# Performance work log

Measured on AMD Instinct MI355X. Metric: run time of the kernel, lower is better.

The kernel has to match this reference:

```python
import jax, jax.numpy as jnp
import numpy as np
import math

B, T = 8, 16
CODE_NUM = 1024
CODE_SIZE = 48
GRAPH_SIZE = 32
HIDDEN = 150      # hidden_size == t_output_size
T_ATTN = 32       # t_attention_size
DP_ATTN = 32      # DotProductAttention size
OUT = 1024


def _lin(k, fan_in, fan_out):
    s = 1.0 / math.sqrt(fan_in)
    kw, kb = jax.random.split(k)
    W = jax.random.uniform(kw, (fan_in, fan_out), minval=-s, maxval=s, dtype=jnp.float32)
    b = jax.random.uniform(kb, (fan_out,), minval=-s, maxval=s, dtype=jnp.float32)
    return W, b


def setup_inputs():
    key = jax.random.key(0)
    ks = jax.random.split(key, 16)
    u = jax.random.uniform(ks[0], (B, T, CODE_NUM))
    m1 = (u < 0.03).astype(jnp.float32)                   # persistent codes
    m2 = ((u >= 0.03) & (u < 0.05)).astype(jnp.float32)   # emerging neighbor codes
    m3 = ((u >= 0.05) & (u < 0.06)).astype(jnp.float32)   # emerging unrelated codes
    divided = jnp.stack([m1, m2, m3], axis=-1)            # [B,T,N,3], disjoint
    code_x = jnp.clip(m1 + m2 + m3, 0.0, 1.0)             # current-visit codes
    neighbors = ((u >= 0.06) & (u < 0.12)).astype(jnp.float32)
    lens = jax.random.randint(ks[1], (B,), T // 2, T + 1)
    a = (jax.random.uniform(ks[2], (CODE_NUM, CODE_NUM)) < 0.01).astype(jnp.float32)
    adj = a / (a.sum(axis=1, keepdims=True) + 1e-6)
    c_emb = jax.random.normal(ks[3], (CODE_NUM, CODE_SIZE)) * 0.05
    n_emb = jax.random.normal(ks[4], (CODE_NUM, CODE_SIZE)) * 0.05
    u_emb = jax.random.normal(ks[5], (CODE_NUM, GRAPH_SIZE)) * 0.05
    Wg, bg = _lin(ks[6], CODE_SIZE, GRAPH_SIZE)           # GraphLayer dense
    Wi, bi = _lin(ks[7], GRAPH_SIZE, 3 * HIDDEN)          # GRUCell input (r|z|n)
    Wh, bh = _lin(ks[8], HIDDEN, 3 * HIDDEN)              # GRUCell hidden (r|z|n)
    Wq, bq = _lin(ks[9], GRAPH_SIZE, T_ATTN)
    Wk, bk = _lin(ks[10], GRAPH_SIZE, T_ATTN)
    Wv, bv = _lin(ks[11], GRAPH_SIZE, HIDDEN)
    Wd, bd = _lin(ks[12], HIDDEN, DP_ATTN)                # DotProductAttention dense
    context = jax.random.normal(ks[13], (DP_ATTN,)) * 0.1
    Wc, bc = _lin(ks[14], HIDDEN, OUT)                    # Classifier
    return dict(code_x=code_x, divided=divided, neighbors=neighbors, lens=lens,
                adj=adj, c_emb=c_emb, n_emb=n_emb, u_emb=u_emb, Wg=Wg, bg=bg,
                Wi=Wi, bi=bi, Wh=Wh, bh=bh, Wq=Wq, bq=bq, Wk=Wk, bk=bk,
                Wv=Wv, bv=bv, Wd=Wd, bd=bd, context=context, Wc=Wc, bc=bc)


def _forward(code_x, divided, neighbors, lens, adj, c_emb, n_emb, u_emb,
             Wg, bg, Wi, bi, Wh, bh, Wq, bq, Wk, bk, Wv, bv, Wd, bd, context, Wc, bc):
    Bb, Tt, N = code_x.shape
    H = Wh.shape[0]
    NEG = -1e30
    scale = 1.0 / math.sqrt(Wq.shape[1])

    def step(carry, xs):
        h_prev, no_prev = carry                 # [B,N,H], [B,N,G]
        c_t, d_t, n_t, t_idx = xs               # [B,N], [B,N,3], [B,N], scalar
        c = c_t[..., None]
        nb = n_t[..., None]
        # GraphLayer: masked embeddings + one-hop adjacency aggregation
        ce = c * c_emb                           # [B,N,C]
        ne = nb * n_emb
        adj_ce = jnp.einsum('mn,bnc->bmc', adj, ce)
        adj_ne = jnp.einsum('mn,bnc->bmc', adj, ne)
        co = jax.nn.leaky_relu((ce + c * adj_ce + c * adj_ne) @ Wg + bg)      # [B,N,G]
        no = jax.nn.leaky_relu((ne + nb * adj_ne + nb * adj_ce) @ Wg + bg)

        m1 = d_t[..., 0]; m2 = d_t[..., 1]; m3 = d_t[..., 2]
        # TransitionLayer part 1: GRUCell on persistent (m1) codes; h_new starts at 0
        gi = co @ Wi + bi
        gh = h_prev @ Wh + bh
        i_r, i_z, i_n = jnp.split(gi, 3, axis=-1)
        h_r, h_z, h_n = jnp.split(gh, 3, axis=-1)
        r = jax.nn.sigmoid(i_r + h_r)
        z = jax.nn.sigmoid(i_z + h_z)
        n_g = jnp.tanh(i_n + r * h_n)
        h_m1 = (1.0 - z) * n_g + z * h_prev
        h_new = jnp.where(m1[..., None] > 0, h_m1, 0.0)

        # TransitionLayer part 2: single-head attention over emerging (m2|m3) codes, t>0
        m23 = (m2 + m3) > 0
        qrows = jnp.where(m2[..., None] > 0, no_prev,
                          jnp.where(m3[..., None] > 0, u_emb, 0.0))           # [B,N,G]
        q = qrows @ Wq + bq
        k = co @ Wk + bk
        v = qrows @ Wv + bv
        s = jnp.einsum('bia,bja->bij', q, k) * scale
        s = jnp.where(m23[:, None, :], s, NEG)   # keys restricted to m2|m3 set
        h_m23 = jnp.tanh(jnp.einsum('bij,bjh->bih', jax.nn.softmax(s, axis=-1), v))
        use23 = t_idx > 0
        h_new = jnp.where(jnp.logical_and(use23, m23)[..., None], h_m23, h_new)

        # per-step output: max-pool over each active subset (0 if subset empty)
        om1 = jnp.max(jnp.where(m1[..., None] > 0, h_m1, NEG), axis=1)
        om1 = jnp.where(jnp.any(m1 > 0, axis=1)[:, None], om1, 0.0)
        om23 = jnp.max(jnp.where(m23[..., None], h_m23, NEG), axis=1)
        om23 = jnp.where(jnp.logical_and(use23, jnp.any(m23, axis=1))[:, None], om23, 0.0)
        return (h_new, no), om1 + om23

    h0 = jnp.zeros((Bb, N, H), code_x.dtype)
    no0 = jnp.zeros((Bb, N, Wg.shape[1]), code_x.dtype)
    xs = (jnp.moveaxis(code_x, 1, 0), jnp.moveaxis(divided, 1, 0),
          jnp.moveaxis(neighbors, 1, 0), jnp.arange(Tt))
    _, outs = jax.lax.scan(step, (h0, no0), xs)
    outs = jnp.moveaxis(outs, 0, 1)              # [B,T,H]

    # DotProductAttention over (ragged) visit axis
    vu = (outs @ Wd + bd) @ context              # [B,T]
    tmask = jnp.arange(Tt)[None, :] < lens[:, None]
    score = jax.nn.softmax(jnp.where(tmask, vu, NEG), axis=-1)
    pooled = jnp.einsum('bth,bt->bh', outs, score)
    # Classifier (dropout_rate=0 -> identity) with sigmoid activation
    return jax.nn.sigmoid(pooled @ Wc + bc)


def reference(code_x, divided, neighbors, lens, adj, c_emb, n_emb, u_emb,
              Wg, bg, Wi, bi, Wh, bh, Wq, bq, Wk, bk, Wv, bv, Wd, bd, context, Wc, bc):
    return _forward(code_x, divided, neighbors, lens, adj, c_emb, n_emb, u_emb,
                    Wg, bg, Wi, bi, Wh, bh, Wq, bq, Wk, bk, Wv, bv, Wd, bd,
                    context, Wc, bc)
```

## Files before the change

kernel.cpp:

```cpp
#include <hip/hip_runtime.h>
#include <hip/hip_bf16.h>

#define Bq   8
#define Tq   16
#define Nq   1024
#define Cq   48
#define Gq   32
#define Hq   150
#define H3q  450
#define TAq  32
#define OUTq 1024
#define BTq  128

#define NC_CAP 128
#define NM_CAP 64
#define NACT   (2 * NC_CAP)
#define MTILE  16
#define NMH    (NM_CAP / 2)

__device__ __forceinline__ float lrelu(float x){ return x > 0.f ? x : 0.01f * x; }
__device__ __forceinline__ float sigm(float x){ return 1.f / (1.f + expf(-x)); }

__device__ int   g_n1[BTq], g_n23[BTq], g_nchain[BTq], g_nchain2[BTq];
__device__ short g_list1[BTq][NM_CAP];
__device__ short g_list23[BTq][NM_CAP];
__device__ short g_mapc[BTq][Nq];
__device__ short g_mapn[BTq][Nq];
__device__ int   g_chain[BTq][NM_CAP];
__device__ int   g_chain2[BTq][NM_CAP];
__device__ unsigned char g_cls[BTq][NM_CAP];
__device__ float g_Pc[Nq][Gq];
__device__ float g_Pn[Nq][Gq];
__device__ float g_co[BTq][NC_CAP][Gq];
__device__ float g_no[BTq][NC_CAP][Gq];
__device__ float g_hm23[BTq][NM_CAP][Hq];
__device__ float g_om23p2[2][BTq][Hq];
__device__ float g_hm1[BTq][NM_CAP][Hq];
__device__ float g_om1p2[2][BTq][Hq];
__device__ float g_om1c[BTq][Hq];

__device__ __forceinline__ void gi3(const float* co_row, const float* Wi, const float* bi, int h,
                                    float& gr, float& gz, float& gn){
    gr = bi[h]; gz = bi[Hq + h]; gn = bi[2 * Hq + h];
    #pragma unroll
    for (int g = 0; g < Gq; ++g){
        float c = co_row[g];
        const float* w = Wi + g * H3q + h;
        gr += c * w[0];
        gz += c * w[Hq];
        gn += c * w[2 * Hq];
    }
}

__global__ __launch_bounds__(256) void k_pre(const float* c_emb, const float* n_emb, const float* Wg){
    int idx   = blockIdx.x * 256 + threadIdx.x;
    int which = idx >> 15;
    int r     = (idx >> 5) & 1023;
    int g     = idx & 31;
    const float* emb = which ? n_emb : c_emb;
    float acc = 0.f;
    for (int c = 0; c < Cq; ++c)
        acc += emb[r * Cq + c] * Wg[c * Gq + g];
    if (which) g_Pn[r][g] = acc; else g_Pc[r][g] = acc;
}

__global__ __launch_bounds__(512) void k_co(const float* code_x, const float* neighbors,
                                            const float* adj, const float* bg){
    int bt = blockIdx.x >> 1, half = blockIdx.x & 1, tid = threadIdx.x;
    __shared__ unsigned char cf_s[Nq], nf_s[Nq];
    __shared__ short lc_s[NC_CAP], ln_s[NC_CAP];
    __shared__ short act_s[NACT];
    __shared__ int nc_s, nn_s;
    __shared__ float Pact_s[NACT][Gq];
    __shared__ float A_s[MTILE][NACT];
    __shared__ short mrow_s[MTILE];
    int wave = tid >> 6, lane = tid & 63;

    for (int n = tid; n < Nq; n += 512){
        cf_s[n] = (code_x[bt * Nq + n]    > 0.f) ? 1 : 0;
        nf_s[n] = (neighbors[bt * Nq + n] > 0.f) ? 1 : 0;
    }
    __syncthreads();
    if (wave == 0){
        int base = 0;
        for (int start = 0; start < Nq; start += 64){
            int n = start + lane;
            int pred = cf_s[n];
            unsigned long long mm = __ballot(pred != 0);
            int pos = base + (int)__popcll(mm & ((1ull << lane) - 1ull));
            if (pred && pos < NC_CAP) lc_s[pos] = (short)n;
            base += (int)__popcll(mm);
        }
        if (lane == 0) nc_s = min(base, NC_CAP);
    } else if (wave == 1){
        int base = 0;
        for (int start = 0; start < Nq; start += 64){
            int n = start + lane;
            int pred = nf_s[n];
            unsigned long long mm = __ballot(pred != 0);
            int pos = base + (int)__popcll(mm & ((1ull << lane) - 1ull));
            if (pred && pos < NC_CAP) ln_s[pos] = (short)n;
            base += (int)__popcll(mm);
        }
        if (lane == 0) nn_s = min(base, NC_CAP);
    } else {
        if (half == 0) for (int n = tid - 128; n < Nq; n += 384) g_mapc[bt][n] = -1;
        else           for (int n = tid - 128; n < Nq; n += 384) g_mapn[bt][n] = -1;
    }
    __syncthreads();
    int nc = nc_s, nn = nn_s, total = nc + nn;

    for (int i = tid; i < total; i += 512) act_s[i] = (i < nc) ? lc_s[i] : ln_s[i - nc];
    if (half == 0) for (int i = tid; i < nc; i += 512) g_mapc[bt][lc_s[i]] = (short)i;
    else           for (int i = tid; i < nn; i += 512) g_mapn[bt][ln_s[i]] = (short)i;
    __syncthreads();

    for (int idx = tid; idx < total * Gq; idx += 512){
        int i = idx >> 5, g = idx & 31;
        Pact_s[i][g] = (i < nc) ? g_Pc[act_s[i]][g] : g_Pn[act_s[i]][g];
    }
    __syncthreads();

    int g = tid & 31, grp = tid >> 5;
    float bgv = bg[g];
    for (int rbase = half; rbase < total; rbase += 2 * MTILE){
        if (tid < MTILE){
            int r = rbase + 2 * tid;
            mrow_s[tid] = (r < total) ? act_s[r] : 0;
        }
        __syncthreads();
        int ntile = min(MTILE, (total - rbase + 1) / 2);
        for (int idx = tid; idx < ntile * total; idx += 512){
            int ti = idx / total, j = idx % total;
            A_s[ti][j] = adj[(size_t)mrow_s[ti] * Nq + act_s[j]];
        }
        __syncthreads();
        if (grp < ntile){
            int r = rbase + 2 * grp;
            float agg = 0.f;
            #pragma unroll 4
            for (int j = 0; j < total; ++j) agg += A_s[grp][j] * Pact_s[j][g];
            float v = lrelu(Pact_s[r][g] + agg + bgv);
            if (r < nc) g_co[bt][r][g]      = v;
            else        g_no[bt][r - nc][g] = v;
        }
        __syncthreads();
    }
}

__global__ __launch_bounds__(512) void k_mid(const float* divided, const float* u_emb,
                                             const float* Wk, const float* bk,
                                             const float* Wq_, const float* bq_,
                                             const float* Wv_, const float* bv_,
                                             const float* bg){
    int bt = blockIdx.x >> 1, half = blockIdx.x & 1, tid = threadIdx.x;
    int t = bt % Tq, btp = bt - 1;
    __shared__ unsigned char f1_s[Nq], f2_s[Nq], f3_s[Nq];
    __shared__ short l1_s[NM_CAP], l23_s[NM_CAP];
    __shared__ unsigned char wm_s[NMH];
    __shared__ int n1_s, n23_s;
    __shared__ float co23_s[NM_CAP][Gq];
    __shared__ float qr_s[NM_CAP][Gq];
    __shared__ float q_s[NMH][TAq + 1];
    __shared__ float k_s[NM_CAP][TAq + 1];
    __shared__ float s_s[NMH][NM_CAP + 1];
    __shared__ float vv_s[NM_CAP][Hq];
    __shared__ float hm_s[NMH][Hq];
    int wave = tid >> 6, lane = tid & 63;

    for (int idx = tid; idx < Nq * 3; idx += 512){
        float v = divided[(size_t)bt * Nq * 3 + idx];
        int n = idx / 3, c = idx - n * 3;
        unsigned char f = (v > 0.f) ? 1 : 0;
        if (c == 0) f1_s[n] = f;
        else if (c == 1) f2_s[n] = f;
        else f3_s[n] = f;
    }
    __syncthreads();
    if (wave == 0){
        int base = 0;
        for (int start = 0; start < Nq; start += 64){
            int n = start + lane;
            int pred = f1_s[n];
            unsigned long long mm = __ballot(pred != 0);
            int pos = base + (int)__popcll(mm & ((1ull << lane) - 1ull));
            if (pred && pos < NM_CAP) l1_s[pos] = (short)n;
            base += (int)__popcll(mm);
        }
        if (lane == 0) n1_s = min(base, NM_CAP);
    } else if (wave == 1){
        int base = 0;
        for (int start = 0; start < Nq; start += 64){
            int n = start + lane;
            int m2 = f2_s[n], m3 = f3_s[n];
            int pred = m2 | m3;
            unsigned long long mm = __ballot(pred != 0);
            int pos = base + (int)__popcll(mm & ((1ull << lane) - 1ull));
            if (pred && pos < NM_CAP) l23_s[pos] = (short)(n | (m2 ? 0x400 : 0));
            base += (int)__popcll(mm);
        }
        if (lane == 0) n23_s = min(base, NM_CAP);
    }
    __syncthreads();
    int n1 = n1_s, n23 = n23_s;
    if (half == 0){
        for (int i = tid; i < n1;  i += 512) g_list1[bt][i]  = l1_s[i];
        for (int i = tid; i < n23; i += 512) g_list23[bt][i] = l23_s[i];
        if (tid == 0){ g_n1[bt] = n1; g_n23[bt] = n23; }
    }
    if (t == 0 || n23 == 0) return;
    int nMy = (n23 > half) ? ((n23 - half + 1) >> 1) : 0;

    for (int il = tid; il < nMy; il += 512){
        int row = l23_s[2 * il + half] & 1023;
        unsigned char wm = 0;
        if (t < Tq - 1) wm = (divided[((size_t)(bt + 1) * Nq + row) * 3] > 0.f) ? 1 : 0;
        wm_s[il] = wm;
    }
    for (int idx = tid; idx < n23 * Gq; idx += 512){
        int i = idx >> 5, g = idx & 31;
        co23_s[i][g] = g_co[bt][g_mapc[bt][l23_s[i] & 1023]][g];
    }
    for (int idx = tid; idx < n23 * Gq; idx += 512){
        int i = idx >> 5, g = idx & 31;
        int e = l23_s[i], row = e & 1023;
        float qv;
        if (e & 0x400){
            int slot = g_mapn[btp][row];
            qv = (slot >= 0) ? g_no[btp][slot][g] : lrelu(bg[g]);
        } else {
            qv = u_emb[row * Gq + g];
        }
        qr_s[i][g] = qv;
    }
    __syncthreads();
    for (int idx = tid; idx < n23 * TAq; idx += 512){
        int i = idx >> 5, a = idx & 31;
        float acck = bk[a];
        #pragma unroll
        for (int g = 0; g < Gq; ++g) acck += co23_s[i][g] * Wk[g * TAq + a];
        k_s[i][a] = acck;
    }
    for (int idx = tid; idx < nMy * TAq; idx += 512){
        int il = idx >> 5, a = idx & 31;
        int i = 2 * il + half;
        float accq = bq_[a];
        #pragma unroll
        for (int g = 0; g < Gq; ++g) accq += qr_s[i][g] * Wq_[g * TAq + a];
        q_s[il][a] = accq;
    }
    for (int idx = tid; idx < n23 * Hq; idx += 512){
        int i = idx / Hq, h = idx % Hq;
        float acc = bv_[h];
        #pragma unroll
        for (int g = 0; g < Gq; ++g) acc += qr_s[i][g] * Wv_[g * Hq + h];
        vv_s[i][h] = acc;
    }
    __syncthreads();

    const float scale = 0.17677669529663687f;
    for (int idx = tid; idx < nMy * n23; idx += 512){
        int il = idx / n23, j = idx % n23;
        float acc = 0.f;
        #pragma unroll
        for (int a = 0; a < TAq; ++a) acc += q_s[il][a] * k_s[j][a];
        s_s[il][j] = acc * scale;
    }
    __syncthreads();
    for (int il = tid; il < nMy; il += 512){
        float mx = -1e30f;
        for (int j = 0; j < n23; ++j) mx = fmaxf(mx, s_s[il][j]);
        float sum = 0.f;
        for (int j = 0; j < n23; ++j){ float e = expf(s_s[il][j] - mx); s_s[il][j] = e; sum += e; }
        float inv = 1.f / sum;
        for (int j = 0; j < n23; ++j) s_s[il][j] *= inv;
    }
    __syncthreads();
    for (int idx = tid; idx < nMy * Hq; idx += 512){
        int il = idx / Hq, h = idx % Hq;
        float acc = 0.f;
        for (int j = 0; j < n23; ++j) acc += s_s[il][j] * vv_s[j][h];
        hm_s[il][h] = tanhf(acc);
    }
    __syncthreads();
    for (int idx = tid; idx < nMy * Hq; idx += 512){
        int il = idx / Hq, h = idx % Hq;
        if (wm_s[il]) g_hm23[bt][2 * il + half][h] = hm_s[il][h];
    }
    for (int h = tid; h < Hq; h += 512){
        float mx = -1e30f;
        for (int il = 0; il < nMy; ++il) mx = fmaxf(mx, hm_s[il][h]);
        g_om23p2[half][bt][h] = mx;
    }
}

__global__ __launch_bounds__(512) void k_gru1(const float* Wi, const float* bi,
                                              const float* Wh, const float* bh){
    int bt = blockIdx.x >> 1, half = blockIdx.x & 1, tid = threadIdx.x;
    int t = bt % Tq, btp = bt - 1;
    __shared__ short map1p[Nq], map23p[Nq];
    __shared__ short l1_s[NM_CAP];
    __shared__ unsigned char cls_s[NM_CAP];
    __shared__ int m23l_s[NM_CAP];
    __shared__ int nf23_s;
    __shared__ float co1_s[NMH][Gq];
    __shared__ float hb_s[Hq];
    __shared__ float ghf_s[H3q];
    __shared__ float gi_s[NMH][H3q];
    int n1 = g_n1[bt];
    int nMy = (n1 > half) ? ((n1 - half + 1) >> 1) : 0;
    for (int n = tid; n < Nq; n += 512){ map1p[n] = -1; map23p[n] = -1; }
    for (int i = tid; i < n1; i += 512) l1_s[i] = g_list1[bt][i];
    __syncthreads();
    if (t >= 1){
        int n1p = g_n1[btp];
        for (int i = tid; i < n1p; i += 512) map1p[g_list1[btp][i]] = (short)i;
        if (t >= 2){
            int n23p = g_n23[btp];
            for (int i = tid; i < n23p; i += 512) map23p[g_list23[btp][i] & 1023] = (short)i;
        }
    }
    __syncthreads();
    if (tid < 64){
        int i = tid;
        int cls = 0, sp = -1;
        if (i < n1 && t >= 1){
            int row = l1_s[i];
            if (map1p[row] >= 0){ cls = 1; sp = map1p[row]; }
            else if (t >= 2 && map23p[row] >= 0){ cls = 2; sp = map23p[row]; }
        }
        if (i < n1) cls_s[i] = (unsigned char)cls;
        if (half == 0 && i < n1) g_cls[bt][i] = (unsigned char)cls;
        unsigned long long mch = __ballot(cls == 1);
        unsigned long long m23 = __ballot(cls == 2 && (i & 1) == half);
        int pch = (int)__popcll(mch & ((1ull << i) - 1ull));
        int p23 = (int)__popcll(m23 & ((1ull << i) - 1ull));
        if (half == 0 && cls == 1) g_chain[bt][pch] = (i << 16) | sp;
        if (cls == 2 && (i & 1) == half) m23l_s[p23] = (i << 16) | sp;
        if (i == 0){
            nf23_s = (int)__popcll(m23);
            if (half == 0) g_nchain[bt] = (int)__popcll(mch);
        }
    }
    for (int idx = tid; idx < nMy * Gq; idx += 512){
        int il = idx >> 5, g = idx & 31;
        co1_s[il][g] = g_co[bt][g_mapc[bt][l1_s[2 * il + half]]][g];
    }
    __syncthreads();

    if (tid < H3q){
        float wcol[Gq];
        #pragma unroll
        for (int g = 0; g < Gq; ++g) wcol[g] = Wi[g * H3q + tid];
        float bij = bi[tid];
        for (int il = 0; il < nMy; ++il){
            float acc = bij;
            #pragma unroll
            for (int g = 0; g < Gq; ++g) acc += co1_s[il][g] * wcol[g];
            gi_s[il][tid] = acc;
        }
    }
    __syncthreads();

    for (int idx = tid; idx < nMy * Hq; idx += 512){
        int il = idx / Hq, h = idx % Hq;
        int i = 2 * il + half;
        if (cls_s[i] != 0) continue;
        float gr = gi_s[il][h], gz = gi_s[il][Hq + h], gn = gi_s[il][2 * Hq + h];
        float r  = sigm(gr + bh[h]);
        float z  = sigm(gz + bh[Hq + h]);
        float ng = tanhf(gn + r * bh[2 * Hq + h]);
        gi_s[il][h] = (1.f - z) * ng;
    }
    __syncthreads();

    int nf23 = nf23_s;
    for (int f = 0; f < nf23; ++f){
        int pk = m23l_s[f]; int i = pk >> 16, sp = pk & 0xffff;
        int il = i >> 1;
        for (int h = tid; h < Hq; h += 512) hb_s[h] = g_hm23[btp][sp][h];
        __syncthreads();
        for (int j = tid; j < H3q; j += 512){
            float acc = bh[j];
            for (int k2 = 0; k2 < Hq; ++k2) acc += hb_s[k2] * Wh[k2 * H3q + j];
            ghf_s[j] = acc;
        }
        __syncthreads();
        for (int h = tid; h < Hq; h += 512){
            float gr = gi_s[il][h], gz = gi_s[il][Hq + h], gn = gi_s[il][2 * Hq + h];
            float r  = sigm(gr + ghf_s[h]);
            float z  = sigm(gz + ghf_s[Hq + h]);
            float ng = tanhf(gn + r * ghf_s[2 * Hq + h]);
            gi_s[il][h] = (1.f - z) * ng + z * hb_s[h];
        }
        __syncthreads();
    }

    for (int idx = tid; idx < nMy * Hq; idx += 512){
        int il = idx / Hq, h = idx % Hq;
        int i = 2 * il + half;
        if (cls_s[i] != 1) g_hm1[bt][i][h] = gi_s[il][h];
    }
    for (int h = tid; h < Hq; h += 512){
        float mx = -1e30f;
        for (int il = 0; il < nMy; ++il)
            if (cls_s[2 * il + half] != 1) mx = fmaxf(mx, gi_s[il][h]);
        g_om1p2[half][bt][h] = mx;
    }
}

__global__ __launch_bounds__(512) void k_gru1b(const float* Wi, const float* bi,
                                               const float* Wh, const float* bh){
    int bt = blockIdx.x, tid = threadIdx.x;
    int t = bt % Tq, btp = bt - 1;
    __shared__ unsigned char defer_s[NM_CAP];
    __shared__ float co_s[Gq];
    __shared__ float hb_s[Hq];
    __shared__ float ghf_s[H3q];
    __shared__ float cmax_s[Hq];
    int nch = (t > 0) ? g_nchain[bt] : 0;
    for (int h = tid; h < Hq; h += 512) cmax_s[h] = -1e30f;
    if (tid < 64){
        int c = tid;
        int defer = 0;
        if (c < nch){
            int sp = g_chain[bt][c] & 0xffff;
            defer = (g_cls[btp][sp] == 1) ? 1 : 0;
            defer_s[c] = (unsigned char)defer;
        }
        unsigned long long md = __ballot((c < nch) && defer);
        int pos = (int)__popcll(md & ((1ull << c) - 1ull));
        if ((c < nch) && defer) g_chain2[bt][pos] = g_chain[bt][c];
        if (c == 0) g_nchain2[bt] = (int)__popcll(md);
    }
    __syncthreads();
    for (int c = 0; c < nch; ++c){
        if (defer_s[c]) continue;
        int pk = g_chain[bt][c]; int i = pk >> 16, sp = pk & 0xffff;
        if (tid < Gq) co_s[tid] = g_co[bt][g_mapc[bt][g_list1[bt][i]]][tid];
        for (int h = tid; h < Hq; h += 512) hb_s[h] = g_hm1[btp][sp][h];
        __syncthreads();
        for (int j = tid; j < H3q; j += 512){
            float acc = bh[j];
            for (int k2 = 0; k2 < Hq; ++k2) acc += hb_s[k2] * Wh[k2 * H3q + j];
            ghf_s[j] = acc;
        }
        __syncthreads();
        for (int h = tid; h < Hq; h += 512){
            float gr, gz, gn;
            gi3(co_s, Wi, bi, h, gr, gz, gn);
            float r  = sigm(gr + ghf_s[h]);
            float z  = sigm(gz + ghf_s[Hq + h]);
            float ng = tanhf(gn + r * ghf_s[2 * Hq + h]);
            float v  = (1.f - z) * ng + z * hb_s[h];
            g_hm1[bt][i][h] = v;
            cmax_s[h] = fmaxf(cmax_s[h], v);
        }
        __syncthreads();
    }
    for (int h = tid; h < Hq; h += 512) g_om1c[bt][h] = cmax_s[h];
}

__global__ __launch_bounds__(512) void k_gru2f(const float* Wi, const float* bi,
                                               const float* Wh, const float* bh,
                                               const int* lens, const float* Wd, const float* bd,
                                               const float* ctx, const float* Wc, const float* bc,
                                               float* out){
    int b = blockIdx.x, tid = threadIdx.x;
    __shared__ float co_s[Gq];
    __shared__ float hb_s[Hq];
    __shared__ float ghf_s[H3q];
    __shared__ float outs_s[Tq][Hq];
    __shared__ float wdc_s[Hq];
    __shared__ float score_s[Tq];
    __shared__ float pooled_s[Hq];
    for (int t = 1; t < Tq; ++t){
        int bt = b * Tq + t, btp = bt - 1;
        int nch2 = g_nchain2[bt];
        for (int c = 0; c < nch2; ++c){
            int pk = g_chain2[bt][c]; int i = pk >> 16, sp = pk & 0xffff;
            if (tid < Gq) co_s[tid] = g_co[bt][g_mapc[bt][g_list1[bt][i]]][tid];
            for (int h = tid; h < Hq; h += 512) hb_s[h] = g_hm1[btp][sp][h];
            __syncthreads();
            for (int j = tid; j < H3q; j += 512){
                float acc = bh[j];
                for (int k2 = 0; k2 < Hq; ++k2) acc += hb_s[k2] * Wh[k2 * H3q + j];
                ghf_s[j] = acc;
            }
            __syncthreads();
            for (int h = tid; h < Hq; h += 512){
                float gr, gz, gn;
                gi3(co_s, Wi, bi, h, gr, gz, gn);
                float r  = sigm(gr + ghf_s[h]);
                float z  = sigm(gz + ghf_s[Hq + h]);
                float ng = tanhf(gn + r * ghf_s[2 * Hq + h]);
                g_hm1[bt][i][h] = (1.f - z) * ng + z * hb_s[h];
            }
            __syncthreads();
        }
    }
    for (int idx = tid; idx < Tq * Hq; idx += 512){
        int t = idx / Hq, h = idx % Hq;
        int bt = b * Tq + t;
        int n1 = g_n1[bt], n23 = (t > 0) ? g_n23[bt] : 0;
        float o = 0.f;
        if (n1 > 0){
            float mx = fmaxf(fmaxf(g_om1p2[0][bt][h], g_om1p2[1][bt][h]), g_om1c[bt][h]);
            int nd = (t > 0) ? g_nchain2[bt] : 0;
            for (int c = 0; c < nd; ++c){
                int i = g_chain2[bt][c] >> 16;
                mx = fmaxf(mx, g_hm1[bt][i][h]);
            }
            o = mx;
        }
        if (n23 > 0) o += fmaxf(g_om23p2[0][bt][h], g_om23p2[1][bt][h]);
        outs_s[t][h] = o;
    }
    for (int h = tid; h < Hq; h += 512){
        float acc = 0.f;
        for (int d = 0; d < 32; ++d) acc += Wd[h * 32 + d] * ctx[d];
        wdc_s[h] = acc;
    }
    __syncthreads();
    int len = lens[b];
    if (tid < Tq){
        int t = tid;
        float acc = 0.f;
        for (int d = 0; d < 32; ++d) acc += bd[d] * ctx[d];
        for (int h = 0; h < Hq; ++h) acc += outs_s[t][h] * wdc_s[h];
        score_s[t] = (t < len) ? acc : -1e30f;
    }
    __syncthreads();
    if (tid == 0){
        float mx = -1e30f;
        for (int t = 0; t < Tq; ++t) mx = fmaxf(mx, score_s[t]);
        float sum = 0.f;
        for (int t = 0; t < Tq; ++t){ float e = expf(score_s[t] - mx); score_s[t] = e; sum += e; }
        float inv = 1.f / sum;
        for (int t = 0; t < Tq; ++t) score_s[t] *= inv;
    }
    __syncthreads();
    for (int h = tid; h < Hq; h += 512){
        float acc = 0.f;
        for (int t = 0; t < Tq; ++t) acc += score_s[t] * outs_s[t][h];
        pooled_s[h] = acc;
    }
    __syncthreads();
    for (int o = tid; o < OUTq; o += 512){
        float acc = bc[o];
        for (int h = 0; h < Hq; ++h) acc += pooled_s[h] * Wc[h * OUTq + o];
        out[b * OUTq + o] = sigm(acc);
    }
}

extern "C" void kernel_launch(void* const* d_in, const int* in_sizes, int n_in,
                              void* d_out, int out_size, void* d_ws, size_t ws_size,
                              hipStream_t stream){
    const float* code_x    = (const float*)d_in[0];
    const float* divided   = (const float*)d_in[1];
    const float* neighbors = (const float*)d_in[2];
    const int*   lens      = (const int*)  d_in[3];
    const float* adj       = (const float*)d_in[4];
    const float* c_emb     = (const float*)d_in[5];
    const float* n_emb     = (const float*)d_in[6];
    const float* u_emb     = (const float*)d_in[7];
    const float* Wg        = (const float*)d_in[8];
    const float* bg        = (const float*)d_in[9];
    const float* Wi        = (const float*)d_in[10];
    const float* bi        = (const float*)d_in[11];
    const float* Wh        = (const float*)d_in[12];
    const float* bh        = (const float*)d_in[13];
    const float* Wq_       = (const float*)d_in[14];
    const float* bq_       = (const float*)d_in[15];
    const float* Wk_       = (const float*)d_in[16];
    const float* bk_       = (const float*)d_in[17];
    const float* Wv_       = (const float*)d_in[18];
    const float* bv_       = (const float*)d_in[19];
    const float* Wd_       = (const float*)d_in[20];
    const float* bd_       = (const float*)d_in[21];
    const float* ctx       = (const float*)d_in[22];
    const float* Wc_       = (const float*)d_in[23];
    const float* bc_       = (const float*)d_in[24];
    float* out = (float*)d_out;

    hipLaunchKernelGGL(k_pre,   dim3(256),     dim3(256), 0, stream, c_emb, n_emb, Wg);
    hipLaunchKernelGGL(k_co,    dim3(2 * BTq), dim3(512), 0, stream, code_x, neighbors, adj, bg);
    hipLaunchKernelGGL(k_mid,   dim3(2 * BTq), dim3(512), 0, stream, divided, u_emb,
                       Wk_, bk_, Wq_, bq_, Wv_, bv_, bg);
    hipLaunchKernelGGL(k_gru1,  dim3(2 * BTq), dim3(512), 0, stream, Wi, bi, Wh, bh);
    hipLaunchKernelGGL(k_gru1b, dim3(BTq),     dim3(512), 0, stream, Wi, bi, Wh, bh);
    hipLaunchKernelGGL(k_gru2f, dim3(Bq),      dim3(512), 0, stream, Wi, bi, Wh, bh,
                       lens, Wd_, bd_, ctx, Wc_, bc_, out);
}
```

Measured before the change: 258.5 us.

## Fuse all stages into one cooperative persistent kernel with grid syncs

The six separate kernel launches are replaced by a single cooperative kernel of 256 blocks. The stages are separated by grid.sync(), and each stage's shared memory lives in one union. The goal is to remove per-launch overhead and the gaps between dependent small kernels. In exchange, every stage must run with the same block count and the largest shared-memory footprint. Grid-wide barriers have their own cost, and the final stage leaves most blocks idle.

```diff
diff --git a/kernel.cpp b/kernel.cpp
--- a/kernel.cpp
+++ b/kernel.cpp
@@ -1,5 +1,8 @@
 #include <hip/hip_runtime.h>
 #include <hip/hip_bf16.h>
+#include <hip/hip_cooperative_groups.h>
+
+namespace cg = cooperative_groups;
 
 #define Bq   8
 #define Tq   16
@@ -52,504 +55,513 @@
     }
 }
 
-__global__ __launch_bounds__(256) void k_pre(const float* c_emb, const float* n_emb, const float* Wg){
-    int idx   = blockIdx.x * 256 + threadIdx.x;
-    int which = idx >> 15;
-    int r     = (idx >> 5) & 1023;
-    int g     = idx & 31;
-    const float* emb = which ? n_emb : c_emb;
-    float acc = 0.f;
-    for (int c = 0; c < Cq; ++c)
-        acc += emb[r * Cq + c] * Wg[c * Gq + g];
-    if (which) g_Pn[r][g] = acc; else g_Pc[r][g] = acc;
-}
-
-__global__ __launch_bounds__(512) void k_co(const float* code_x, const float* neighbors,
-                                            const float* adj, const float* bg){
-    int bt = blockIdx.x >> 1, half = blockIdx.x & 1, tid = threadIdx.x;
-    __shared__ unsigned char cf_s[Nq], nf_s[Nq];
-    __shared__ short lc_s[NC_CAP], ln_s[NC_CAP];
-    __shared__ short act_s[NACT];
-    __shared__ int nc_s, nn_s;
-    __shared__ float Pact_s[NACT][Gq];
-    __shared__ float A_s[MTILE][NACT];
-    __shared__ short mrow_s[MTILE];
+struct SmCo {
+    unsigned char cf[Nq], nf[Nq];
+    short lc[NC_CAP], ln[NC_CAP];
+    short act[NACT];
+    int nc, nn;
+    float Pact[NACT][Gq];
+    float A[MTILE][NACT];
+    short mrow[MTILE];
+};
+struct SmMid {
+    unsigned char f1[Nq], f2[Nq], f3[Nq];
+    short l1[NM_CAP], l23[NM_CAP];
+    unsigned char wm[NMH];
+    int n1, n23;
+    float co23[NM_CAP][Gq];
+    float qr[NM_CAP][Gq];
+    float q[NMH][TAq + 1];
+    float k[NM_CAP][TAq + 1];
+    float s[NMH][NM_CAP + 1];
+    float vv[NM_CAP][Hq];
+    float hm[NMH][Hq];
+};
+struct SmG1 {
+    short map1p[Nq], map23p[Nq];
+    short l1[NM_CAP];
+    unsigned char cls[NM_CAP];
+    int m23l[NM_CAP];
+    int nf23;
+    float co1[NMH][Gq];
+    float hb[Hq];
+    float ghf[H3q];
+    float gi[NMH][H3q];
+};
+struct SmG1b {
+    unsigned char defer[NM_CAP];
+    float co[Gq];
+    float hb[Hq];
+    float ghf[H3q];
+    float cmax[Hq];
+};
+struct SmG2f {
+    float co[Gq];
+    float hb[Hq];
+    float ghf[H3q];
+    float outs[Tq][Hq];
+    float wdc[Hq];
+    float score[Tq];
+    float pooled[Hq];
+};
+union SmU { SmCo co; SmMid mid; SmG1 g1; SmG1b g1b; SmG2f g2f; };
+
+__global__ __launch_bounds__(512) void k_fused(
+        const float* code_x, const float* divided, const float* neighbors, const int* lens,
+        const float* adj, const float* c_emb, const float* n_emb, const float* u_emb,
+        const float* Wg, const float* bg, const float* Wi, const float* bi,
+        const float* Wh, const float* bh, const float* Wq_, const float* bq_,
+        const float* Wk_, const float* bk_, const float* Wv_, const float* bv_,
+        const float* Wd_, const float* bd_, const float* ctx, const float* Wc_,
+        const float* bc_, float* out){
+    cg::grid_group grid = cg::this_grid();
+    __shared__ SmU sm;
+    int blk = blockIdx.x, tid = threadIdx.x;
     int wave = tid >> 6, lane = tid & 63;
 
-    for (int n = tid; n < Nq; n += 512){
-        cf_s[n] = (code_x[bt * Nq + n]    > 0.f) ? 1 : 0;
-        nf_s[n] = (neighbors[bt * Nq + n] > 0.f) ? 1 : 0;
+    {
+        int idx = blk * 512 + tid;
+        if (idx < 65536){
+            int which = idx >> 15;
+            int r = (idx >> 5) & 1023;
+            int g = idx & 31;
+            const float* emb = which ? n_emb : c_emb;
+            float acc = 0.f;
+            for (int c = 0; c < Cq; ++c) acc += emb[r * Cq + c] * Wg[c * Gq + g];
+            if (which) g_Pn[r][g] = acc; else g_Pc[r][g] = acc;
+        }
     }
-    __syncthreads();
-    if (wave == 0){
-        int base = 0;
-        for (int start = 0; start < Nq; start += 64){
-            int n = start + lane;
-            int pred = cf_s[n];
-            unsigned long long mm = __ballot(pred != 0);
-            int pos = base + (int)__popcll(mm & ((1ull << lane) - 1ull));
-            if (pred && pos < NC_CAP) lc_s[pos] = (short)n;
-            base += (int)__popcll(mm);
-        }
-        if (lane == 0) nc_s = min(base, NC_CAP);
-    } else if (wave == 1){
-        int base = 0;
-        for (int start = 0; start < Nq; start += 64){
-            int n = start + lane;
-            int pred = nf_s[n];
-            unsigned long long mm = __ballot(pred != 0);
-            int pos = base + (int)__popcll(mm & ((1ull << lane) - 1ull));
-            if (pred && pos < NC_CAP) ln_s[pos] = (short)n;
-            base += (int)__popcll(mm);
-        }
-        if (lane == 0) nn_s = min(base, NC_CAP);
-    } else {
-        if (half == 0) for (int n = tid - 128; n < Nq; n += 384) g_mapc[bt][n] = -1;
-        else           for (int n = tid - 128; n < Nq; n += 384) g_mapn[bt][n] = -1;
+    grid.sync();
+
+    {
+        int bt = blk >> 1, half = blk & 1;
+        for (int n = tid; n < Nq; n += 512){
+            sm.co.cf[n] = (code_x[bt * Nq + n]    > 0.f) ? 1 : 0;
+            sm.co.nf[n] = (neighbors[bt * Nq + n] > 0.f) ? 1 : 0;
+        }
+        __syncthreads();
+        if (wave == 0){
+            int base = 0;
+            for (int start = 0; start < Nq; start += 64){
+                int n = start + lane;
+                int pred = sm.co.cf[n];
+                unsigned long long mm = __ballot(pred != 0);
+                int pos = base + (int)__popcll(mm & ((1ull << lane) - 1ull));
+                if (pred && pos < NC_CAP) sm.co.lc[pos] = (short)n;
+                base += (int)__popcll(mm);
+            }
+            if (lane == 0) sm.co.nc = min(base, NC_CAP);
+        } else if (wave == 1){
+            int base = 0;
+            for (int start = 0; start < Nq; start += 64){
+                int n = start + lane;
+                int pred = sm.co.nf[n];
+                unsigned long long mm = __ballot(pred != 0);
+                int pos = base + (int)__popcll(mm & ((1ull << lane) - 1ull));
+                if (pred && pos < NC_CAP) sm.co.ln[pos] = (short)n;
+                base += (int)__popcll(mm);
+            }
+            if (lane == 0) sm.co.nn = min(base, NC_CAP);
+        } else {
+            if (half == 0) for (int n = tid - 128; n < Nq; n += 384) g_mapc[bt][n] = -1;
+            else           for (int n = tid - 128; n < Nq; n += 384) g_mapn[bt][n] = -1;
+        }
+        __syncthreads();
+        int nc = sm.co.nc, nn = sm.co.nn, total = nc + nn;
+        for (int i = tid; i < total; i += 512) sm.co.act[i] = (i < nc) ? sm.co.lc[i] : sm.co.ln[i - nc];
+        if (half == 0) for (int i = tid; i < nc; i += 512) g_mapc[bt][sm.co.lc[i]] = (short)i;
+        else           for (int i = tid; i < nn; i += 512) g_mapn[bt][sm.co.ln[i]] = (short)i;
+        __syncthreads();
+        for (int idx = tid; idx < total * Gq; idx += 512){
+            int i = idx >> 5, g = idx & 31;
+            sm.co.Pact[i][g] = (i < nc) ? g_Pc[sm.co.act[i]][g] : g_Pn[sm.co.act[i]][g];
+        }
+        __syncthreads();
+        int g = tid & 31, grp = tid >> 5;
+        float bgv = bg[g];
+        for (int rbase = half; rbase < total; rbase += 2 * MTILE){
+            if (tid < MTILE){
+                int r = rbase + 2 * tid;
+                sm.co.mrow[tid] = (r < total) ? sm.co.act[r] : 0;
+            }
+            __syncthreads();
+            int ntile = min(MTILE, (total - rbase + 1) / 2);
+            for (int idx = tid; idx < ntile * total; idx += 512){
+                int ti = idx / total, j = idx % total;
+                sm.co.A[ti][j] = adj[(size_t)sm.co.mrow[ti] * Nq + sm.co.act[j]];
+            }
+            __syncthreads();
+            if (grp < ntile){
+                int r = rbase + 2 * grp;
+                float agg = 0.f;
+                #pragma unroll 4
+                for (int j = 0; j < total; ++j) agg += sm.co.A[grp][j] * sm.co.Pact[j][g];
+                float v = lrelu(sm.co.Pact[r][g] + agg + bgv);
+                if (r < nc) g_co[bt][r][g]      = v;
+                else        g_no[bt][r - nc][g] = v;
+            }
+            __syncthreads();
+        }
     }
-    __syncthreads();
-    int nc = nc_s, nn = nn_s, total = nc + nn;
-
-    for (int i = tid; i < total; i += 512) act_s[i] = (i < nc) ? lc_s[i] : ln_s[i - nc];
-    if (half == 0) for (int i = tid; i < nc; i += 512) g_mapc[bt][lc_s[i]] = (short)i;
-    else           for (int i = tid; i < nn; i += 512) g_mapn[bt][ln_s[i]] = (short)i;
-    __syncthreads();
-
-    for (int idx = tid; idx < total * Gq; idx += 512){
-        int i = idx >> 5, g = idx & 31;
-        Pact_s[i][g] = (i < nc) ? g_Pc[act_s[i]][g] : g_Pn[act_s[i]][g];
+    grid.sync();
+
+    {
+        int bt = blk >> 1, half = blk & 1;
+        int t = bt % Tq, btp = bt - 1;
+        for (int idx = tid; idx < Nq * 3; idx += 512){
+            float v = divided[(size_t)bt * Nq * 3 + idx];
+            int n = idx / 3, c = idx - n * 3;
+            unsigned char f = (v > 0.f) ? 1 : 0;
+            if (c == 0) sm.mid.f1[n] = f;
+            else if (c == 1) sm.mid.f2[n] = f;
+            else sm.mid.f3[n] = f;
+        }
+        __syncthreads();
+        if (wave == 0){
+            int base = 0;
+            for (int start = 0; start < Nq; start += 64){
+                int n = start + lane;
+                int pred = sm.mid.f1[n];
+                unsigned long long mm = __ballot(pred != 0);
+                int pos = base + (int)__popcll(mm & ((1ull << lane) - 1ull));
+                if (pred && pos < NM_CAP) sm.mid.l1[pos] = (short)n;
+                base += (int)__popcll(mm);
+            }
+            if (lane == 0) sm.mid.n1 = min(base, NM_CAP);
+        } else if (wave == 1){
+            int base = 0;
+            for (int start = 0; start < Nq; start += 64){
+                int n = start + lane;
+                int m2 = sm.mid.f2[n], m3 = sm.mid.f3[n];
+                int pred = m2 | m3;
+                unsigned long long mm = __ballot(pred != 0);
+                int pos = base + (int)__popcll(mm & ((1ull << lane) - 1ull));
+                if (pred && pos < NM_CAP) sm.mid.l23[pos] = (short)(n | (m2 ? 0x400 : 0));
+                base += (int)__popcll(mm);
+            }
+            if (lane == 0) sm.mid.n23 = min(base, NM_CAP);
+        }
+        __syncthreads();
+        int n1 = sm.mid.n1, n23 = sm.mid.n23;
+        if (half == 0){
+            for (int i = tid; i < n1;  i += 512) g_list1[bt][i]  = sm.mid.l1[i];
+            for (int i = tid; i < n23; i += 512) g_list23[bt][i] = sm.mid.l23[i];
+            if (tid == 0){ g_n1[bt] = n1; g_n23[bt] = n23; }
+        }
+        if (t != 0 && n23 != 0){
+            int nMy = (n23 > half) ? ((n23 - half + 1) >> 1) : 0;
+            for (int il = tid; il < nMy; il += 512){
+                int row = sm.mid.l23[2 * il + half] & 1023;
+                unsigned char wm = 0;
+                if (t < Tq - 1) wm = (divided[((size_t)(bt + 1) * Nq + row) * 3] > 0.f) ? 1 : 0;
+                sm.mid.wm[il] = wm;
+            }
+            for (int idx = tid; idx < n23 * Gq; idx += 512){
+                int i = idx >> 5, g = idx & 31;
+                sm.mid.co23[i][g] = g_co[bt][g_mapc[bt][sm.mid.l23[i] & 1023]][g];
+            }
+            for (int idx = tid; idx < n23 * Gq; idx += 512){
+                int i = idx >> 5, g = idx & 31;
+                int e = sm.mid.l23[i], row = e & 1023;
+                float qv;
+                if (e & 0x400){
+                    int slot = g_mapn[btp][row];
+                    qv = (slot >= 0) ? g_no[btp][slot][g] : lrelu(bg[g]);
+                } else {
+                    qv = u_emb[row * Gq + g];
+                }
+                sm.mid.qr[i][g] = qv;
+            }
+            __syncthreads();
+            for (int idx = tid; idx < n23 * TAq; idx += 512){
+                int i = idx >> 5, a = idx & 31;
+                float acck = bk_[a];
+                #pragma unroll
+                for (int g = 0; g < Gq; ++g) acck += sm.mid.co23[i][g] * Wk_[g * TAq + a];
+                sm.mid.k[i][a] = acck;
+            }
+            for (int idx = tid; idx < nMy * TAq; idx += 512){
+                int il = idx >> 5, a = idx & 31;
+                int i = 2 * il + half;
+                float accq = bq_[a];
+                #pragma unroll
+                for (int g = 0; g < Gq; ++g) accq += sm.mid.qr[i][g] * Wq_[g * TAq + a];
+                sm.mid.q[il][a] = accq;
+            }
+            for (int idx = tid; idx < n23 * Hq; idx += 512){
+                int i = idx / Hq, h = idx % Hq;
+                float acc = bv_[h];
+                #pragma unroll
+                for (int g = 0; g < Gq; ++g) acc += sm.mid.qr[i][g] * Wv_[g * Hq + h];
+                sm.mid.vv[i][h] = acc;
+            }
+            __syncthreads();
+            const float scale = 0.17677669529663687f;
+            for (int idx = tid; idx < nMy * n23; idx += 512){
+                int il = idx / n23, j = idx % n23;
+                float acc = 0.f;
+                #pragma unroll
+                for (int a = 0; a < TAq; ++a) acc += sm.mid.q[il][a] * sm.mid.k[j][a];
+                sm.mid.s[il][j] = acc * scale;
+            }
+            __syncthreads();
+            for (int il = tid; il < nMy; il += 512){
+                float mx = -1e30f;
+                for (int j = 0; j < n23; ++j) mx = fmaxf(mx, sm.mid.s[il][j]);
+                float sum = 0.f;
+                for (int j = 0; j < n23; ++j){ float e = expf(sm.mid.s[il][j] - mx); sm.mid.s[il][j] = e; sum += e; }
+                float inv = 1.f / sum;
+                for (int j = 0; j < n23; ++j) sm.mid.s[il][j] *= inv;
+            }
+            __syncthreads();
+            for (int idx = tid; idx < nMy * Hq; idx += 512){
+                int il = idx / Hq, h = idx % Hq;
+                float acc = 0.f;
+                for (int j = 0; j < n23; ++j) acc += sm.mid.s[il][j] * sm.mid.vv[j][h];
+                sm.mid.hm[il][h] = tanhf(acc);
+            }
+            __syncthreads();
+            for (int idx = tid; idx < nMy * Hq; idx += 512){
+                int il = idx / Hq, h = idx % Hq;
+                if (sm.mid.wm[il]) g_hm23[bt][2 * il + half][h] = sm.mid.hm[il][h];
+            }
+            for (int h = tid; h < Hq; h += 512){
+                float mx = -1e30f;
+                for (int il = 0; il < nMy; ++il) mx = fmaxf(mx, sm.mid.hm[il][h]);
+                g_om23p2[half][bt][h] = mx;
+            }
+        }
     }
-    __syncthreads();
-
-    int g = tid & 31, grp = tid >> 5;
-    float bgv = bg[g];
-    for (int rbase = half; rbase < total; rbase += 2 * MTILE){
-        if (tid < MTILE){
-            int r = rbase + 2 * tid;
-            mrow_s[tid] = (r < total) ? act_s[r] : 0;
-        }
-        __syncthreads();
-        int ntile = min(MTILE, (total - rbase + 1) / 2);
-        for (int idx = tid; idx < ntile * total; idx += 512){
-            int ti = idx / total, j = idx % total;
-            A_s[ti][j] = adj[(size_t)mrow_s[ti] * Nq + act_s[j]];
-        }
-        __syncthreads();
-        if (grp < ntile){
-            int r = rbase + 2 * grp;
-            float agg = 0.f;
-            #pragma unroll 4
-            for (int j = 0; j < total; ++j) agg += A_s[grp][j] * Pact_s[j][g];
-            float v = lrelu(Pact_s[r][g] + agg + bgv);
-            if (r < nc) g_co[bt][r][g]      = v;
-            else        g_no[bt][r - nc][g] = v;
-        }
-        __syncthreads();
-    }
-}
-
-__global__ __launch_bounds__(512) void k_mid(const float* divided, const float* u_emb,
-                                             const float* Wk, const float* bk,
-                                             const float* Wq_, const float* bq_,
-                                             const float* Wv_, const float* bv_,
-                                             const float* bg){
-    int bt = blockIdx.x >> 1, half = blockIdx.x & 1, tid = threadIdx.x;
-    int t = bt % Tq, btp = bt - 1;
-    __shared__ unsigned char f1_s[Nq], f2_s[Nq], f3_s[Nq];
-    __shared__ short l1_s[NM_CAP], l23_s[NM_CAP];
-    __shared__ unsigned char wm_s[NMH];
-    __shared__ int n1_s, n23_s;
-    __shared__ float co23_s[NM_CAP][Gq];
-    __shared__ float qr_s[NM_CAP][Gq];
-    __shared__ float q_s[NMH][TAq + 1];
-    __shared__ float k_s[NM_CAP][TAq + 1];
-    __shared__ float s_s[NMH][NM_CAP + 1];
-    __shared__ float vv_s[NM_CAP][Hq];
-    __shared__ float hm_s[NMH][Hq];
-    int wave = tid >> 6, lane = tid & 63;
-
-    for (int idx = tid; idx < Nq * 3; idx += 512){
-        float v = divided[(size_t)bt * Nq * 3 + idx];
-        int n = idx / 3, c = idx - n * 3;
-        unsigned char f = (v > 0.f) ? 1 : 0;
-        if (c == 0) f1_s[n] = f;
-        else if (c == 1) f2_s[n] = f;
-        else f3_s[n] = f;
-    }
-    __syncthreads();
-    if (wave == 0){
-        int base = 0;
-        for (int start = 0; start < Nq; start += 64){
-            int n = start + lane;
-            int pred = f1_s[n];
-            unsigned long long mm = __ballot(pred != 0);
-            int pos = base + (int)__popcll(mm & ((1ull << lane) - 1ull));
-            if (pred && pos < NM_CAP) l1_s[pos] = (short)n;
-            base += (int)__popcll(mm);
-        }
-        if (lane == 0) n1_s = min(base, NM_CAP);
-    } else if (wave == 1){
-        int base = 0;
-        for (int start = 0; start < Nq; start += 64){
-            int n = start + lane;
-            int m2 = f2_s[n], m3 = f3_s[n];
-            int pred = m2 | m3;
-            unsigned long long mm = __ballot(pred != 0);
-            int pos = base + (int)__popcll(mm & ((1ull << lane) - 1ull));
-            if (pred && pos < NM_CAP) l23_s[pos] = (short)(n | (m2 ? 0x400 : 0));
-            base += (int)__popcll(mm);
-        }
-        if (lane == 0) n23_s = min(base, NM_CAP);
-    }
-    __syncthreads();
-    int n1 = n1_s, n23 = n23_s;
-    if (half == 0){
-        for (int i = tid; i < n1;  i += 512) g_list1[bt][i]  = l1_s[i];
-        for (int i = tid; i < n23; i += 512) g_list23[bt][i] = l23_s[i];
-        if (tid == 0){ g_n1[bt] = n1; g_n23[bt] = n23; }
-    }
-    if (t == 0 || n23 == 0) return;
-    int nMy = (n23 > half) ? ((n23 - half + 1) >> 1) : 0;
-
-    for (int il = tid; il < nMy; il += 512){
-        int row = l23_s[2 * il + half] & 1023;
-        unsigned char wm = 0;
-        if (t < Tq - 1) wm = (divided[((size_t)(bt + 1) * Nq + row) * 3] > 0.f) ? 1 : 0;
-        wm_s[il] = wm;
-    }
-    for (int idx = tid; idx < n23 * Gq; idx += 512){
-        int i = idx >> 5, g = idx & 31;
-        co23_s[i][g] = g_co[bt][g_mapc[bt][l23_s[i] & 1023]][g];
-    }
-    for (int idx = tid; idx < n23 * Gq; idx += 512){
-        int i = idx >> 5, g = idx & 31;
-        int e = l23_s[i], row = e & 1023;
-        float qv;
-        if (e & 0x400){
-            int slot = g_mapn[btp][row];
-            qv = (slot >= 0) ? g_no[btp][slot][g] : lrelu(bg[g]);
-        } else {
-            qv = u_emb[row * Gq + g];
-        }
-        qr_s[i][g] = qv;
-    }
-    __syncthreads();
-    for (int idx = tid; idx < n23 * TAq; idx += 512){
-        int i = idx >> 5, a = idx & 31;
-        float acck = bk[a];
-        #pragma unroll
-        for (int g = 0; g < Gq; ++g) acck += co23_s[i][g] * Wk[g * TAq + a];
-        k_s[i][a] = acck;
-    }
-    for (int idx = tid; idx < nMy * TAq; idx += 512){
-        int il = idx >> 5, a = idx & 31;
-        int i = 2 * il + half;
-        float accq = bq_[a];
-        #pragma unroll
-        for (int g = 0; g < Gq; ++g) accq += qr_s[i][g] * Wq_[g * TAq + a];
-        q_s[il][a] = accq;
-    }
-    for (int idx = tid; idx < n23 * Hq; idx += 512){
-        int i = idx / Hq, h = idx % Hq;
-        float acc = bv_[h];
-        #pragma unroll
-        for (int g = 0; g < Gq; ++g) acc += qr_s[i][g] * Wv_[g * Hq + h];
-        vv_s[i][h] = acc;
-    }
-    __syncthreads();
-
-    const float scale = 0.17677669529663687f;
-    for (int idx = tid; idx < nMy * n23; idx += 512){
-        int il = idx / n23, j = idx % n23;
-        float acc = 0.f;
-        #pragma unroll
-        for (int a = 0; a < TAq; ++a) acc += q_s[il][a] * k_s[j][a];
-        s_s[il][j] = acc * scale;
-    }
-    __syncthreads();
-    for (int il = tid; il < nMy; il += 512){
-        float mx = -1e30f;
-        for (int j = 0; j < n23; ++j) mx = fmaxf(mx, s_s[il][j]);
-        float sum = 0.f;
-        for (int j = 0; j < n23; ++j){ float e = expf(s_s[il][j] - mx); s_s[il][j] = e; sum += e; }
-        float inv = 1.f / sum;
-        for (int j = 0; j < n23; ++j) s_s[il][j] *= inv;
-    }
-    __syncthreads();
-    for (int idx = tid; idx < nMy * Hq; idx += 512){
-        int il = idx / Hq, h = idx % Hq;
-        float acc = 0.f;
-        for (int j = 0; j < n23; ++j) acc += s_s[il][j] * vv_s[j][h];
-        hm_s[il][h] = tanhf(acc);
-    }
-    __syncthreads();
-    for (int idx = tid; idx < nMy * Hq; idx += 512){
-        int il = idx / Hq, h = idx % Hq;
-        if (wm_s[il]) g_hm23[bt][2 * il + half][h] = hm_s[il][h];
-    }
-    for (int h = tid; h < Hq; h += 512){
-        float mx = -1e30f;
-        for (int il = 0; il < nMy; ++il) mx = fmaxf(mx, hm_s[il][h]);
-        g_om23p2[half][bt][h] = mx;
-    }
-}
-
-__global__ __launch_bounds__(512) void k_gru1(const float* Wi, const float* bi,
-                                              const float* Wh, const float* bh){
-    int bt = blockIdx.x >> 1, half = blockIdx.x & 1, tid = threadIdx.x;
-    int t = bt % Tq, btp = bt - 1;
-    __shared__ short map1p[Nq], map23p[Nq];
-    __shared__ short l1_s[NM_CAP];
-    __shared__ unsigned char cls_s[NM_CAP];
-    __shared__ int m23l_s[NM_CAP];
-    __shared__ int nf23_s;
-    __shared__ float co1_s[NMH][Gq];
-    __shared__ float hb_s[Hq];
-    __shared__ float ghf_s[H3q];
-    __shared__ float gi_s[NMH][H3q];
-    int n1 = g_n1[bt];
-    int nMy = (n1 > half) ? ((n1 - half + 1) >> 1) : 0;
-    for (int n = tid; n < Nq; n += 512){ map1p[n] = -1; map23p[n] = -1; }
-    for (int i = tid; i < n1; i += 512) l1_s[i] = g_list1[bt][i];
-    __syncthreads();
-    if (t >= 1){
-        int n1p = g_n1[btp];
-        for (int i = tid; i < n1p; i += 512) map1p[g_list1[btp][i]] = (short)i;
-        if (t >= 2){
-            int n23p = g_n23[btp];
-            for (int i = tid; i < n23p; i += 512) map23p[g_list23[btp][i] & 1023] = (short)i;
-        }
-    }
-    __syncthreads();
-    if (tid < 64){
-        int i = tid;
-        int cls = 0, sp = -1;
-        if (i < n1 && t >= 1){
-            int row = l1_s[i];
-            if (map1p[row] >= 0){ cls = 1; sp = map1p[row]; }
-            else if (t >= 2 && map23p[row] >= 0){ cls = 2; sp = map23p[row]; }
-        }
-        if (i < n1) cls_s[i] = (unsigned char)cls;
-        if (half == 0 && i < n1) g_cls[bt][i] = (unsigned char)cls;
-        unsigned long long mch = __ballot(cls == 1);
-        unsigned long long m23 = __ballot(cls == 2 && (i & 1) == half);
-        int pch = (int)__popcll(mch & ((1ull << i) - 1ull));
-        int p23 = (int)__popcll(m23 & ((1ull << i) - 1ull));
-        if (half == 0 && cls == 1) g_chain[bt][pch] = (i << 16) | sp;
-        if (cls == 2 && (i & 1) == half) m23l_s[p23] = (i << 16) | sp;
-        if (i == 0){
-            nf23_s = (int)__popcll(m23);
-            if (half == 0) g_nchain[bt] = (int)__popcll(mch);
-        }
-    }
-    for (int idx = tid; idx < nMy * Gq; idx += 512){
-        int il = idx >> 5, g = idx & 31;
-        co1_s[il][g] = g_co[bt][g_mapc[bt][l1_s[2 * il + half]]][g];
-    }
-    __syncthreads();
-
-    if (tid < H3q){
-        float wcol[Gq];
-        #pragma unroll
-        for (int g = 0; g < Gq; ++g) wcol[g] = Wi[g * H3q + tid];
-        float bij = bi[tid];
-        for (int il = 0; il < nMy; ++il){
-            float acc = bij;
+    grid.sync();
+
+    {
+        int bt = blk >> 1, half = blk & 1;
+        int t = bt % Tq, btp = bt - 1;
+        int n1 = g_n1[bt];
+        int nMy = (n1 > half) ? ((n1 - half + 1) >> 1) : 0;
+        for (int n = tid; n < Nq; n += 512){ sm.g1.map1p[n] = -1; sm.g1.map23p[n] = -1; }
+        for (int i = tid; i < n1; i += 512) sm.g1.l1[i] = g_list1[bt][i];
+        __syncthreads();
+        if (t >= 1){
+            int n1p = g_n1[btp];
+            for (int i = tid; i < n1p; i += 512) sm.g1.map1p[g_list1[btp][i]] = (short)i;
+            if (t >= 2){
+                int n23p = g_n23[btp];
+                for (int i = tid; i < n23p; i += 512) sm.g1.map23p[g_list23[btp][i] & 1023] = (short)i;
+            }
+        }
+        __syncthreads();
+        if (tid < 64){
+            int i = tid;
+            int cls = 0, sp = -1;
+            if (i < n1 && t >= 1){
+                int row = sm.g1.l1[i];
+                if (sm.g1.map1p[row] >= 0){ cls = 1; sp = sm.g1.map1p[row]; }
+                else if (t >= 2 && sm.g1.map23p[row] >= 0){ cls = 2; sp = sm.g1.map23p[row]; }
+            }
+            if (i < n1) sm.g1.cls[i] = (unsigned char)cls;
+            if (half == 0 && i < n1) g_cls[bt][i] = (unsigned char)cls;
+            unsigned long long mch = __ballot(cls == 1);
+            unsigned long long m23 = __ballot(cls == 2 && (i & 1) == half);
+            int pch = (int)__popcll(mch & ((1ull << i) - 1ull));
+            int p23 = (int)__popcll(m23 & ((1ull << i) - 1ull));
+            if (half == 0 && cls == 1) g_chain[bt][pch] = (i << 16) | sp;
+            if (cls == 2 && (i & 1) == half) sm.g1.m23l[p23] = (i << 16) | sp;
+            if (i == 0){
+                sm.g1.nf23 = (int)__popcll(m23);
+                if (half == 0) g_nchain[bt] = (int)__popcll(mch);
+            }
+        }
+        for (int idx = tid; idx < nMy * Gq; idx += 512){
+            int il = idx >> 5, g = idx & 31;
+            sm.g1.co1[il][g] = g_co[bt][g_mapc[bt][sm.g1.l1[2 * il + half]]][g];
+        }
+        __syncthreads();
+        if (tid < H3q){
+            float wcol[Gq];
             #pragma unroll
-            for (int g = 0; g < Gq; ++g) acc += co1_s[il][g] * wcol[g];
-            gi_s[il][tid] = acc;
-        }
-    }
-    __syncthreads();
-
-    for (int idx = tid; idx < nMy * Hq; idx += 512){
-        int il = idx / Hq, h = idx % Hq;
-        int i = 2 * il + half;
-        if (cls_s[i] != 0) continue;
-        float gr = gi_s[il][h], gz = gi_s[il][Hq + h], gn = gi_s[il][2 * Hq + h];
-        float r  = sigm(gr + bh[h]);
-        float z  = sigm(gz + bh[Hq + h]);
-        float ng = tanhf(gn + r * bh[2 * Hq + h]);
-        gi_s[il][h] = (1.f - z) * ng;
-    }
-    __syncthreads();
-
-    int nf23 = nf23_s;
-    for (int f = 0; f < nf23; ++f){
-        int pk = m23l_s[f]; int i = pk >> 16, sp = pk & 0xffff;
-        int il = i >> 1;
-        for (int h = tid; h < Hq; h += 512) hb_s[h] = g_hm23[btp][sp][h];
-        __syncthreads();
-        for (int j = tid; j < H3q; j += 512){
-            float acc = bh[j];
-            for (int k2 = 0; k2 < Hq; ++k2) acc += hb_s[k2] * Wh[k2 * H3q + j];
-            ghf_s[j] = acc;
-        }
-        __syncthreads();
-        for (int h = tid; h < Hq; h += 512){
-            float gr = gi_s[il][h], gz = gi_s[il][Hq + h], gn = gi_s[il][2 * Hq + h];
-            float r  = sigm(gr + ghf_s[h]);
-            float z  = sigm(gz + ghf_s[Hq + h]);
-            float ng = tanhf(gn + r * ghf_s[2 * Hq + h]);
-            gi_s[il][h] = (1.f - z) * ng + z * hb_s[h];
-        }
-        __syncthreads();
-    }
-
-    for (int idx = tid; idx < nMy * Hq; idx += 512){
-        int il = idx / Hq, h = idx % Hq;
-        int i = 2 * il + half;
-        if (cls_s[i] != 1) g_hm1[bt][i][h] = gi_s[il][h];
-    }
-    for (int h = tid; h < Hq; h += 512){
-        float mx = -1e30f;
-        for (int il = 0; il < nMy; ++il)
-            if (cls_s[2 * il + half] != 1) mx = fmaxf(mx, gi_s[il][h]);
-        g_om1p2[half][bt][h] = mx;
-    }
-}
-
-__global__ __launch_bounds__(512) void k_gru1b(const float* Wi, const float* bi,
-                                               const float* Wh, const float* bh){
-    int bt = blockIdx.x, tid = threadIdx.x;
-    int t = bt % Tq, btp = bt - 1;
-    __shared__ unsigned char defer_s[NM_CAP];
-    __shared__ float co_s[Gq];
-    __shared__ float hb_s[Hq];
-    __shared__ float ghf_s[H3q];
-    __shared__ float cmax_s[Hq];
-    int nch = (t > 0) ? g_nchain[bt] : 0;
-    for (int h = tid; h < Hq; h += 512) cmax_s[h] = -1e30f;
-    if (tid < 64){
-        int c = tid;
-        int defer = 0;
-        if (c < nch){
-            int sp = g_chain[bt][c] & 0xffff;
-            defer = (g_cls[btp][sp] == 1) ? 1 : 0;
-            defer_s[c] = (unsigned char)defer;
-        }
-        unsigned long long md = __ballot((c < nch) && defer);
-        int pos = (int)__popcll(md & ((1ull << c) - 1ull));
-        if ((c < nch) && defer) g_chain2[bt][pos] = g_chain[bt][c];
-        if (c == 0) g_nchain2[bt] = (int)__popcll(md);
-    }
-    __syncthreads();
-    for (int c = 0; c < nch; ++c){
-        if (defer_s[c]) continue;
-        int pk = g_chain[bt][c]; int i = pk >> 16, sp = pk & 0xffff;
-        if (tid < Gq) co_s[tid] = g_co[bt][g_mapc[bt][g_list1[bt][i]]][tid];
-        for (int h = tid; h < Hq; h += 512) hb_s[h] = g_hm1[btp][sp][h];
-        __syncthreads();
-        for (int j = tid; j < H3q; j += 512){
-            float acc = bh[j];
-            for (int k2 = 0; k2 < Hq; ++k2) acc += hb_s[k2] * Wh[k2 * H3q + j];
-            ghf_s[j] = acc;
-        }
-        __syncthreads();
-        for (int h = tid; h < Hq; h += 512){
-            float gr, gz, gn;
-            gi3(co_s, Wi, bi, h, gr, gz, gn);
-            float r  = sigm(gr + ghf_s[h]);
-            float z  = sigm(gz + ghf_s[Hq + h]);
-            float ng = tanhf(gn + r * ghf_s[2 * Hq + h]);
-            float v  = (1.f - z) * ng + z * hb_s[h];
-            g_hm1[bt][i][h] = v;
-            cmax_s[h] = fmaxf(cmax_s[h], v);
-        }
-        __syncthreads();
-    }
-    for (int h = tid; h < Hq; h += 512) g_om1c[bt][h] = cmax_s[h];
-}
-
-__global__ __launch_bounds__(512) void k_gru2f(const float* Wi, const float* bi,
-                                               const float* Wh, const float* bh,
-                                               const int* lens, const float* Wd, const float* bd,
-                                               const float* ctx, const float* Wc, const float* bc,
-                                               float* out){
-    int b = blockIdx.x, tid = threadIdx.x;
-    __shared__ float co_s[Gq];
-    __shared__ float hb_s[Hq];
-    __shared__ float ghf_s[H3q];
-    __shared__ float outs_s[Tq][Hq];
-    __shared__ float wdc_s[Hq];
-    __shared__ float score_s[Tq];
-    __shared__ float pooled_s[Hq];
-    for (int t = 1; t < Tq; ++t){
-        int bt = b * Tq + t, btp = bt - 1;
-        int nch2 = g_nchain2[bt];
-        for (int c = 0; c < nch2; ++c){
-            int pk = g_chain2[bt][c]; int i = pk >> 16, sp = pk & 0xffff;
-            if (tid < Gq) co_s[tid] = g_co[bt][g_mapc[bt][g_list1[bt][i]]][tid];
-            for (int h = tid; h < Hq; h += 512) hb_s[h] = g_hm1[btp][sp][h];
+            for (int g = 0; g < Gq; ++g) wcol[g] = Wi[g * H3q + tid];
+            float bij = bi[tid];
+            for (int il = 0; il < nMy; ++il){
+                float acc = bij;
+                #pragma unroll
+                for (int g = 0; g < Gq; ++g) acc += sm.g1.co1[il][g] * wcol[g];
+                sm.g1.gi[il][tid] = acc;
+            }
+        }
+        __syncthreads();
+        for (int idx = tid; idx < nMy * Hq; idx += 512){
+            int il = idx / Hq, h = idx % Hq;
+            int i = 2 * il + half;
+            if (sm.g1.cls[i] != 0) continue;
+            float gr = sm.g1.gi[il][h], gz = sm.g1.gi[il][Hq + h], gn = sm.g1.gi[il][2 * Hq + h];
+            float r  = sigm(gr + bh[h]);
+            float z  = sigm(gz + bh[Hq + h]);
+            float ng = tanhf(gn + r * bh[2 * Hq + h]);
+            sm.g1.gi[il][h] = (1.f - z) * ng;
+        }
+        __syncthreads();
+        int nf23 = sm.g1.nf23;
+        for (int f = 0; f < nf23; ++f){
+            int pk = sm.g1.m23l[f]; int i = pk >> 16, sp = pk & 0xffff;
+            int il = i >> 1;
+            for (int h = tid; h < Hq; h += 512) sm.g1.hb[h] = g_hm23[btp][sp][h];
             __syncthreads();
             for (int j = tid; j < H3q; j += 512){
                 float acc = bh[j];
-                for (int k2 = 0; k2 < Hq; ++k2) acc += hb_s[k2] * Wh[k2 * H3q + j];
-                ghf_s[j] = acc;
+                for (int k2 = 0; k2 < Hq; ++k2) acc += sm.g1.hb[k2] * Wh[k2 * H3q + j];
+                sm.g1.ghf[j] = acc;
+            }
+            __syncthreads();
+            for (int h = tid; h < Hq; h += 512){
+                float gr = sm.g1.gi[il][h], gz = sm.g1.gi[il][Hq + h], gn = sm.g1.gi[il][2 * Hq + h];
+                float r  = sigm(gr + sm.g1.ghf[h]);
+                float z  = sigm(gz + sm.g1.ghf[Hq + h]);
+                float ng = tanhf(gn + r * sm.g1.ghf[2 * Hq + h]);
+                sm.g1.gi[il][h] = (1.f - z) * ng + z * sm.g1.hb[h];
+            }
+            __syncthreads();
+        }
+        for (int idx = tid; idx < nMy * Hq; idx += 512){
+            int il = idx / Hq, h = idx % Hq;
+            int i = 2 * il + half;
+            if (sm.g1.cls[i] != 1) g_hm1[bt][i][h] = sm.g1.gi[il][h];
+        }
+        for (int h = tid; h < Hq; h += 512){
+            float mx = -1e30f;
+            for (int il = 0; il < nMy; ++il)
+                if (sm.g1.cls[2 * il + half] != 1) mx = fmaxf(mx, sm.g1.gi[il][h]);
+            g_om1p2[half][bt][h] = mx;
+        }
+    }
+    grid.sync();
+
+    if (blk < BTq){
+        int bt = blk;
+        int t = bt % Tq, btp = bt - 1;
+        int nch = (t > 0) ? g_nchain[bt] : 0;
+        for (int h = tid; h < Hq; h += 512) sm.g1b.cmax[h] = -1e30f;
+        if (tid < 64){
+            int c = tid;
+            int defer = 0;
+            if (c < nch){
+                int sp = g_chain[bt][c] & 0xffff;
+                defer = (g_cls[btp][sp] == 1) ? 1 : 0;
+                sm.g1b.defer[c] = (unsigned char)defer;
+            }
+            unsigned long long md = __ballot((c < nch) && defer);
+            int pos = (int)__popcll(md & ((1ull << c) - 1ull));
+            if ((c < nch) && defer) g_chain2[bt][pos] = g_chain[bt][c];
+            if (c == 0) g_nchain2[bt] = (int)__popcll(md);
+        }
+        __syncthreads();
+        for (int c = 0; c < nch; ++c){
+            if (sm.g1b.defer[c]) continue;
+            int pk = g_chain[bt][c]; int i = pk >> 16, sp = pk & 0xffff;
+            if (tid < Gq) sm.g1b.co[tid] = g_co[bt][g_mapc[bt][g_list1[bt][i]]][tid];
+            for (int h = tid; h < Hq; h += 512) sm.g1b.hb[h] = g_hm1[btp][sp][h];
+            __syncthreads();
+            for (int j = tid; j < H3q; j += 512){
+                float acc = bh[j];
+                for (int k2 = 0; k2 < Hq; ++k2) acc += sm.g1b.hb[k2] * Wh[k2 * H3q + j];
+                sm.g1b.ghf[j] = acc;
             }
             __syncthreads();
             for (int h = tid; h < Hq; h += 512){
                 float gr, gz, gn;
-                gi3(co_s, Wi, bi, h, gr, gz, gn);
-                float r  = sigm(gr + ghf_s[h]);
-                float z  = sigm(gz + ghf_s[Hq + h]);
-                float ng = tanhf(gn + r * ghf_s[2 * Hq + h]);
-                g_hm1[bt][i][h] = (1.f - z) * ng + z * hb_s[h];
-            }
-            __syncthreads();
-        }
+                gi3(sm.g1b.co, Wi, bi, h, gr, gz, gn);
+                float r  = sigm(gr + sm.g1b.ghf[h]);
+                float z  = sigm(gz + sm.g1b.ghf[Hq + h]);
+                float ng = tanhf(gn + r * sm.g1b.ghf[2 * Hq + h]);
+                float v  = (1.f - z) * ng + z * sm.g1b.hb[h];
+                g_hm1[bt][i][h] = v;
+                sm.g1b.cmax[h] = fmaxf(sm.g1b.cmax[h], v);
+            }
+            __syncthreads();
+        }
+        for (int h = tid; h < Hq; h += 512) g_om1c[bt][h] = sm.g1b.cmax[h];
     }
-    for (int idx = tid; idx < Tq * Hq; idx += 512){
-        int t = idx / Hq, h = idx % Hq;
-        int bt = b * Tq + t;
-        int n1 = g_n1[bt], n23 = (t > 0) ? g_n23[bt] : 0;
-        float o = 0.f;
-        if (n1 > 0){
-            float mx = fmaxf(fmaxf(g_om1p2[0][bt][h], g_om1p2[1][bt][h]), g_om1c[bt][h]);
-            int nd = (t > 0) ? g_nchain2[bt] : 0;
-            for (int c = 0; c < nd; ++c){
-                int i = g_chain2[bt][c] >> 16;
-                mx = fmaxf(mx, g_hm1[bt][i][h]);
-            }
-            o = mx;
-        }
-        if (n23 > 0) o += fmaxf(g_om23p2[0][bt][h], g_om23p2[1][bt][h]);
-        outs_s[t][h] = o;
-    }
-    for (int h = tid; h < Hq; h += 512){
-        float acc = 0.f;
-        for (int d = 0; d < 32; ++d) acc += Wd[h * 32 + d] * ctx[d];
-        wdc_s[h] = acc;
-    }
-    __syncthreads();
-    int len = lens[b];
-    if (tid < Tq){
-        int t = tid;
-        float acc = 0.f;
-        for (int d = 0; d < 32; ++d) acc += bd[d] * ctx[d];
-        for (int h = 0; h < Hq; ++h) acc += outs_s[t][h] * wdc_s[h];
-        score_s[t] = (t < len) ? acc : -1e30f;
-    }
-    __syncthreads();
-    if (tid == 0){
-        float mx = -1e30f;
-        for (int t = 0; t < Tq; ++t) mx = fmaxf(mx, score_s[t]);
-        float sum = 0.f;
-        for (int t = 0; t < Tq; ++t){ float e = expf(score_s[t] - mx); score_s[t] = e; sum += e; }
-        float inv = 1.f / sum;
-        for (int t = 0; t < Tq; ++t) score_s[t] *= inv;
-    }
-    __syncthreads();
-    for (int h = tid; h < Hq; h += 512){
-        float acc = 0.f;
-        for (int t = 0; t < Tq; ++t) acc += score_s[t] * outs_s[t][h];
-        pooled_s[h] = acc;
-    }
-    __syncthreads();
-    for (int o = tid; o < OUTq; o += 512){
-        float acc = bc[o];
-        for (int h = 0; h < Hq; ++h) acc += pooled_s[h] * Wc[h * OUTq + o];
-        out[b * OUTq + o] = sigm(acc);
+    grid.sync();
+
+    if (blk < Bq){
+        int b = blk;
+        for (int t = 1; t < Tq; ++t){
+            int bt = b * Tq + t, btp = bt - 1;
+            int nch2 = g_nchain2[bt];
+            for (int c = 0; c < nch2; ++c){
+                int pk = g_chain2[bt][c]; int i = pk >> 16, sp = pk & 0xffff;
+                if (tid < Gq) sm.g2f.co[tid] = g_co[bt][g_mapc[bt][g_list1[bt][i]]][tid];
+                for (int h = tid; h < Hq; h += 512) sm.g2f.hb[h] = g_hm1[btp][sp][h];
+                __syncthreads();
+                for (int j = tid; j < H3q; j += 512){
+                    float acc = bh[j];
+                    for (int k2 = 0; k2 < Hq; ++k2) acc += sm.g2f.hb[k2] * Wh[k2 * H3q + j];
+                    sm.g2f.ghf[j] = acc;
+                }
+                __syncthreads();
+                for (int h = tid; h < Hq; h += 512){
+                    float gr, gz, gn;
+                    gi3(sm.g2f.co, Wi, bi, h, gr, gz, gn);
+                    float r  = sigm(gr + sm.g2f.ghf[h]);
+                    float z  = sigm(gz + sm.g2f.ghf[Hq + h]);
+                    float ng = tanhf(gn + r * sm.g2f.ghf[2 * Hq + h]);
+                    g_hm1[bt][i][h] = (1.f - z) * ng + z * sm.g2f.hb[h];
+                }
+                __syncthreads();
+            }
+        }
+        for (int idx = tid; idx < Tq * Hq; idx += 512){
+            int t = idx / Hq, h = idx % Hq;
+            int bt = b * Tq + t;
+            int n1 = g_n1[bt], n23 = (t > 0) ? g_n23[bt] : 0;
+            float o = 0.f;
+            if (n1 > 0){
+                float mx = fmaxf(fmaxf(g_om1p2[0][bt][h], g_om1p2[1][bt][h]), g_om1c[bt][h]);
+                int nd = (t > 0) ? g_nchain2[bt] : 0;
+                for (int c = 0; c < nd; ++c){
+                    int i = g_chain2[bt][c] >> 16;
+                    mx = fmaxf(mx, g_hm1[bt][i][h]);
+                }
+                o = mx;
+            }
+            if (n23 > 0) o += fmaxf(g_om23p2[0][bt][h], g_om23p2[1][bt][h]);
+            sm.g2f.outs[t][h] = o;
+        }
+        for (int h = tid; h < Hq; h += 512){
+            float acc = 0.f;
+            for (int d = 0; d < 32; ++d) acc += Wd_[h * 32 + d] * ctx[d];
+            sm.g2f.wdc[h] = acc;
+        }
+        __syncthreads();
+        int len = lens[b];
+        if (tid < Tq){
+            int t = tid;
+            float acc = 0.f;
+            for (int d = 0; d < 32; ++d) acc += bd_[d] * ctx[d];
+            for (int h = 0; h < Hq; ++h) acc += sm.g2f.outs[t][h] * sm.g2f.wdc[h];
+            sm.g2f.score[t] = (t < len) ? acc : -1e30f;
+        }
+        __syncthreads();
+        if (tid == 0){
+            float mx = -1e30f;
+            for (int t = 0; t < Tq; ++t) mx = fmaxf(mx, sm.g2f.score[t]);
+            float sum = 0.f;
+            for (int t = 0; t < Tq; ++t){ float e = expf(sm.g2f.score[t] - mx); sm.g2f.score[t] = e; sum += e; }
+            float inv = 1.f / sum;
+            for (int t = 0; t < Tq; ++t) sm.g2f.score[t] *= inv;
+        }
+        __syncthreads();
+        for (int h = tid; h < Hq; h += 512){
+            float acc = 0.f;
+            for (int t = 0; t < Tq; ++t) acc += sm.g2f.score[t] * sm.g2f.outs[t][h];
+            sm.g2f.pooled[h] = acc;
+        }
+        __syncthreads();
+        for (int o = tid; o < OUTq; o += 512){
+            float acc = bc_[o];
+            for (int h = 0; h < Hq; ++h) acc += sm.g2f.pooled[h] * Wc_[h * OUTq + o];
+            out[b * OUTq + o] = sigm(acc);
+        }
     }
 }
 
@@ -583,12 +595,15 @@
     const float* bc_       = (const float*)d_in[24];
     float* out = (float*)d_out;
 
-    hipLaunchKernelGGL(k_pre,   dim3(256),     dim3(256), 0, stream, c_emb, n_emb, Wg);
-    hipLaunchKernelGGL(k_co,    dim3(2 * BTq), dim3(512), 0, stream, code_x, neighbors, adj, bg);
-    hipLaunchKernelGGL(k_mid,   dim3(2 * BTq), dim3(512), 0, stream, divided, u_emb,
-                       Wk_, bk_, Wq_, bq_, Wv_, bv_, bg);
-    hipLaunchKernelGGL(k_gru1,  dim3(2 * BTq), dim3(512), 0, stream, Wi, bi, Wh, bh);
-    hipLaunchKernelGGL(k_gru1b, dim3(BTq),     dim3(512), 0, stream, Wi, bi, Wh, bh);
-    hipLaunchKernelGGL(k_gru2f, dim3(Bq),      dim3(512), 0, stream, Wi, bi, Wh, bh,
-                       lens, Wd_, bd_, ctx, Wc_, bc_, out);
+    void* args[] = {
+        (void*)&code_x, (void*)&divided, (void*)&neighbors, (void*)&lens,
+        (void*)&adj, (void*)&c_emb, (void*)&n_emb, (void*)&u_emb,
+        (void*)&Wg, (void*)&bg, (void*)&Wi, (void*)&bi,
+        (void*)&Wh, (void*)&bh, (void*)&Wq_, (void*)&bq_,
+        (void*)&Wk_, (void*)&bk_, (void*)&Wv_, (void*)&bv_,
+        (void*)&Wd_, (void*)&bd_, (void*)&ctx, (void*)&Wc_,
+        (void*)&bc_, (void*)&out
+    };
+    hipLaunchCooperativeKernel((const void*)k_fused, dim3(2 * BTq), dim3(512),
+                               args, 0, stream);
 }
```

After: 413.9 us. +60.1%, slower.
